# Kernel optimization log

Hardware: AMD Instinct MI355X
Metric: run time of the kernel (lower is better)

## Reference

```python
import jax, jax.numpy as jnp
import numpy as np

N = 100000      # nodes
E = 1600000     # edges
NG = 512        # graphs in batch
FIN = 7         # in_features
HID = 128       # hidden_channels
OUT = 2         # outfeatures


def setup_inputs() -> dict:
    key = jax.random.key(0)
    ks = jax.random.split(key, 16)
    x = jax.random.normal(ks[0], (N, FIN), jnp.float32)
    edge_index = jax.random.randint(ks[1], (2, E), 0, N, dtype=jnp.int64)
    batch = jnp.sort(jax.random.randint(ks[2], (N,), 0, NG, dtype=jnp.int64))

    def lin_w(k, fan_in, fan_out):
        # glorot-ish init, scale irrelevant for correctness baseline
        return jax.random.normal(k, (fan_in, fan_out), jnp.float32) / np.sqrt(fan_in).astype(np.float32)

    W1 = lin_w(ks[3], FIN, HID); b1 = jnp.zeros((HID,), jnp.float32)
    W2 = lin_w(ks[4], HID, HID); b2 = jnp.zeros((HID,), jnp.float32)
    W3 = lin_w(ks[5], HID, HID); b3 = jnp.zeros((HID,), jnp.float32)
    W4 = lin_w(ks[6], HID, HID); b4 = jnp.zeros((HID,), jnp.float32)
    Wlin = lin_w(ks[7], HID, OUT); blin = jnp.zeros((OUT,), jnp.float32)
    return dict(x=x, edge_index=edge_index, batch=batch,
                W1=W1, b1=b1, W2=W2, b2=b2, W3=W3, b3=b3, W4=W4, b4=b4,
                Wlin=Wlin, blin=blin)


def gcn_conv(h, W, b, src, dst, n):
    # PyG GCNConv: h' = D^{-1/2} (A + I) D^{-1/2} (h W) + b
    # src/dst already include self-loops
    h = h @ W
    deg = jax.ops.segment_sum(jnp.ones(src.shape[0], h.dtype), dst, num_segments=n)
    dinv = jnp.where(deg > 0, jax.lax.rsqrt(deg), jnp.zeros_like(deg))
    norm = dinv[src] * dinv[dst]                       # [E+N]
    agg = jax.ops.segment_sum(norm[:, None] * h[src], dst, num_segments=n)
    return agg + b


def reference(x, edge_index, batch, W1, b1, W2, b2, W3, b3, W4, b4, Wlin, blin):
    loop = jnp.arange(N, dtype=edge_index.dtype)
    src = jnp.concatenate([edge_index[0], loop])       # add self-loops
    dst = jnp.concatenate([edge_index[1], loop])

    h = gcn_conv(x, W1, b1, src, dst, N)
    for W, b in ((W2, b2), (W3, b3), (W4, b4)):
        h = jax.nn.relu(h)
        h = gcn_conv(h, W, b, src, dst, N)

    # global mean pool per graph
    sums = jax.ops.segment_sum(h, batch, num_segments=NG)
    cnt = jax.ops.segment_sum(jnp.ones((N,), h.dtype), batch, num_segments=NG)
    pooled = sums / jnp.maximum(cnt, 1.0)[:, None]     # [NG, HID]

    # dropout is identity in eval mode
    return pooled @ Wlin + blin                        # [NG, OUT]
```

## Files before the change

### kernel.cpp

```cpp
#include <hip/hip_runtime.h>
#include <hip/hip_bf16.h>

#define N_NODES 100000
#define E_EDGES 1600000
#define NG 512
#define FIN 7
#define HID 128
#define NBUCK 782
#define NBLK_SC 256
#define CHUNK 6250
#define TLEN (NBUCK * NBLK_SC)
#define NCH 196
#define MMX_GRID 782
#define AGGW_GRID 25000
#define L1_GRID 25000

typedef __attribute__((ext_vector_type(8))) short bf16x8;
typedef __attribute__((ext_vector_type(4))) float f32x4;

__device__ __forceinline__ float bf_lo(unsigned int u) { return __uint_as_float(u << 16); }
__device__ __forceinline__ float bf_hi(unsigned int u) { return __uint_as_float(u & 0xffff0000u); }
__device__ __forceinline__ unsigned int f2bf_rne(float f) {
    unsigned int x = __float_as_uint(f);
    return (x + 0x7fffu + ((x >> 16) & 1u)) >> 16;
}
__device__ __forceinline__ unsigned int pack_bf2(float lo, float hi) {
    return f2bf_rne(lo) | (f2bf_rne(hi) << 16);
}


__global__ __launch_bounds__(256) void k_hist2(const int* __restrict__ eidx,
                                               int* __restrict__ table,
                                               const float* __restrict__ W4,
                                               const float* __restrict__ b4,
                                               const float* __restrict__ Wlin,
                                               const float* __restrict__ blin,
                                               float* __restrict__ Wc,
                                               float* __restrict__ bc,
                                               float* __restrict__ pooled,
                                               const float* __restrict__ W2,
                                               const float* __restrict__ W3,
                                               unsigned short* __restrict__ WT2,
                                               unsigned short* __restrict__ WT3) {
    __shared__ int h[NBUCK];
    int blk = blockIdx.x, t = threadIdx.x;
    if (blk >= NBLK_SC) {
        int r = blk - NBLK_SC;
        if (r < 64) {
            float4 z = {0.f, 0.f, 0.f, 0.f};
            *(float4*)&pooled[(r * 256 + t) * 4] = z;
        } else if (r == 64) {
            int k = t >> 1, o = t & 1;
            float acc = 0.f;
            for (int j = 0; j < HID; ++j) acc += W4[k * HID + j] * Wlin[j * 2 + o];
            Wc[k * 2 + o] = acc;
            if (k == 0) {
                float b = blin[o];
                for (int j = 0; j < HID; ++j) b += b4[j] * Wlin[j * 2 + o];
                bc[o] = b;
            }
        } else if (r < 129) {
            int idx = (r - 65) * 256 + t;
            int k = idx >> 7, n = idx & 127;
            WT2[n * 128 + k] = (unsigned short)f2bf_rne(W2[idx]);
        } else {
            int idx = (r - 129) * 256 + t;
            int k = idx >> 7, n = idx & 127;
            WT3[n * 128 + k] = (unsigned short)f2bf_rne(W3[idx]);
        }
        return;
    }
    for (int i = t; i < NBUCK; i += 256) h[i] = 0;
    __syncthreads();
    int e0 = blk * CHUNK, e1 = e0 + CHUNK;
    for (int e = e0 + t; e < e1; e += 256)
        atomicAdd(&h[eidx[E_EDGES + e] >> 7], 1);
    __syncthreads();
    for (int i = t; i < NBUCK; i += 256)
        table[i * NBLK_SC + blk] = h[i];
}

__global__ void k_blocksum(const int* __restrict__ table, int* __restrict__ partial) {
    __shared__ int s[256];
    int b = blockIdx.x, t = threadIdx.x;
    int base = b * 1024;
    int sum = 0;
    for (int i = t; i < 1024; i += 256) {
        int idx = base + i;
        sum += (idx < TLEN) ? table[idx] : 0;
    }
    s[t] = sum; __syncthreads();
    for (int st = 128; st > 0; st >>= 1) {
        if (t < st) s[t] += s[t + st];
        __syncthreads();
    }
    if (t == 0) partial[b] = s[0];
}

__global__ void k_scan_blk(int* __restrict__ partial, int* __restrict__ bucketBase,
                           int* __restrict__ rowptr) {
    __shared__ int s[256];
    int t = threadIdx.x;
    int v = (t < NCH) ? partial[t] : 0;
    s[t] = v; __syncthreads();
    for (int st = 1; st < 256; st <<= 1) {
        int a = (t >= st) ? s[t - st] : 0;
        __syncthreads();
        s[t] += a;
        __syncthreads();
    }
    if (t < NCH) partial[t] = s[t] - v;
    if (t == 0) { bucketBase[NBUCK] = E_EDGES; rowptr[N_NODES] = E_EDGES; }
}

__global__ void k_scan_final(int* __restrict__ table, const int* __restrict__ partial,
                             int* __restrict__ bucketBase) {
    __shared__ int s[1024];
    int b = blockIdx.x, t = threadIdx.x;
    int idx = b * 1024 + t;
    int v = (idx < TLEN) ? table[idx] : 0;
    s[t] = v; __syncthreads();
    for (int st = 1; st < 1024; st <<= 1) {
        int add = (t >= st) ? s[t - st] : 0;
        __syncthreads();
        s[t] += add;
        __syncthreads();
    }
    if (idx < TLEN) {
        int ex = partial[b] + s[t] - v;
        table[idx] = ex;
        if ((idx & (NBLK_SC - 1)) == 0) bucketBase[idx / NBLK_SC] = ex;
    }
}

__global__ __launch_bounds__(256) void k_scatter2(const int* __restrict__ eidx,
                                                  const int* __restrict__ table,
                                                  unsigned int* __restrict__ ebuf) {
    __shared__ int loff[NBUCK];
    int blk = blockIdx.x, t = threadIdx.x;
    for (int i = t; i < NBUCK; i += 256) loff[i] = table[i * NBLK_SC + blk];
    __syncthreads();
    int e0 = blk * CHUNK, e1 = e0 + CHUNK;
    for (int e = e0 + t; e < e1; e += 256) {
        int s = eidx[e];
        int d = eidx[E_EDGES + e];
        int p = atomicAdd(&loff[d >> 7], 1);
        ebuf[p] = ((unsigned int)(d & 127) << 17) | (unsigned int)s;
    }
}

__global__ __launch_bounds__(256) void k_bucket(const unsigned int* __restrict__ ebuf,
                                                const int* __restrict__ bucketBase,
                                                int* __restrict__ rowptr,
                                                float* __restrict__ dinv,
                                                int* __restrict__ col,
                                                const float* __restrict__ x,
                                                float* __restrict__ xs) {
    __shared__ int scnt[128], soff[128], scur[128];
    int b = blockIdx.x, t = threadIdx.x;
    int bbase = bucketBase[b], bend = bucketBase[b + 1];
    if (t < 128) { scnt[t] = 0; scur[t] = 0; }
    __syncthreads();
    for (int e = bbase + t; e < bend; e += 256) {
        unsigned int rec = ebuf[e];
        atomicAdd(&scnt[rec >> 17], 1);
    }
    __syncthreads();
    if (t < 128) soff[t] = scnt[t];
    __syncthreads();
    for (int st = 1; st < 128; st <<= 1) {
        int a = (t < 128 && t >= st) ? soff[t - st] : 0;
        __syncthreads();
        if (t < 128) soff[t] += a;
        __syncthreads();
    }
    float dval = 0.f;
    if (t < 128) {
        int ex = soff[t] - scnt[t];
        int node = b * 128 + t;
        if (node < N_NODES) {
            rowptr[node] = bbase + ex;
            dval = rsqrtf((float)(scnt[t] + 1));
            dinv[node] = dval;
        }
        soff[t] = ex;
    }
    __syncthreads();
    for (int e = bbase + t; e < bend; e += 256) {
        unsigned int rec = ebuf[e];
        int dl = rec >> 17;
        int s = rec & 0x1FFFF;
        int p = bbase + soff[dl] + atomicAdd(&scur[dl], 1);
        col[p] = s;
    }
    if (t < 128) {
        int node = b * 128 + t;
        if (node < N_NODES) {
            float4 v0, v1;
            v0.x = dval * x[node * 7 + 0];
            v0.y = dval * x[node * 7 + 1];
            v0.z = dval * x[node * 7 + 2];
            v0.w = dval * x[node * 7 + 3];
            v1.x = dval * x[node * 7 + 4];
            v1.y = dval * x[node * 7 + 5];
            v1.z = dval * x[node * 7 + 6];
            v1.w = 0.f;
            *(float4*)&xs[node * 8] = v0;
            *(float4*)&xs[node * 8 + 4] = v1;
        }
    }
}


__global__ __launch_bounds__(256) void k_l1(const float* __restrict__ xs,
                                            const float* __restrict__ W1,
                                            const float* __restrict__ b1,
                                            const int* __restrict__ rowptr,
                                            const int* __restrict__ col,
                                            const float* __restrict__ dinv,
                                            unsigned int* __restrict__ g1) {
    __shared__ float w1s[FIN * HID];
    __shared__ float b1s[HID];
    int t = threadIdx.x;
    for (int i = t; i < FIN * HID; i += 256) w1s[i] = W1[i];
    if (t < HID) b1s[t] = b1[t];
    __syncthreads();

    int lane = t & 63, wave = t >> 6;
    int g = lane >> 3, r = lane & 7;
    int node = blockIdx.x * 4 + wave;
    float di = dinv[node];
    float acc = (g == 0) ? xs[node * 8 + r] : 0.f;
    int e0 = rowptr[node], e1 = rowptr[node + 1];

    for (int base = e0; base < e1; base += 64) {
        int m = e1 - base; if (m > 64) m = 64;
        int cv = col[base + lane];
        int j = 0;
        for (; j + 8 <= m; j += 8) {
            int s = __shfl(cv, j + g);
            acc += xs[s * 8 + r];
        }
        if (j < m) {
            int jg = j + g;
            int idx = (jg < m) ? jg : j;
            int s = __shfl(cv, idx);
            float u = xs[s * 8 + r];
            if (jg < m) acc += u;
        }
    }
    acc += __shfl_xor(acc, 8);
    acc += __shfl_xor(acc, 16);
    acc += __shfl_xor(acc, 32);
    acc *= di;

    float av[FIN];
    #pragma unroll
    for (int k = 0; k < FIN; ++k) av[k] = __shfl(acc, k);
    float2 bb = *(const float2*)&b1s[2 * lane];
    float acc0 = bb.x, acc1 = bb.y;
    #pragma unroll
    for (int k = 0; k < FIN; ++k) {
        float2 w = *(const float2*)&w1s[k * HID + 2 * lane];
        acc0 += av[k] * w.x;
        acc1 += av[k] * w.y;
    }
    g1[(size_t)node * 64 + lane] = pack_bf2(di * fmaxf(acc0, 0.f), di * fmaxf(acc1, 0.f));
}


__global__ __launch_bounds__(256) void k_aggW(const unsigned int* __restrict__ gIn,
                                              unsigned int* __restrict__ gOut,
                                              const int* __restrict__ rowptr,
                                              const int* __restrict__ colv,
                                              const float* __restrict__ dinv) {
    int wid = (blockIdx.x * blockDim.x + threadIdx.x) >> 6;
    int lane = threadIdx.x & 63;
    if (wid >= N_NODES) return;
    int i = wid;
    float di = dinv[i];
    int e0 = rowptr[i], e1 = rowptr[i + 1];
    int cv = colv[e0 + lane];
    unsigned int v = gIn[(size_t)i * 64 + lane];
    float ax = bf_lo(v), ay = bf_hi(v);

    for (int base = e0; base < e1; base += 64) {
        int m = e1 - base; if (m > 64) m = 64;
        int cvn = cv;
        if (base + 64 < e1) cvn = colv[base + 64 + lane];
        int j = 0;
        for (; j + 7 < m; j += 8) {
            int s0 = __shfl(cv, j),     s1 = __shfl(cv, j + 1);
            int s2 = __shfl(cv, j + 2), s3 = __shfl(cv, j + 3);
            int s4 = __shfl(cv, j + 4), s5 = __shfl(cv, j + 5);
            int s6 = __shfl(cv, j + 6), s7 = __shfl(cv, j + 7);
            unsigned int u0 = gIn[(size_t)s0 * 64 + lane];
            unsigned int u1 = gIn[(size_t)s1 * 64 + lane];
            unsigned int u2 = gIn[(size_t)s2 * 64 + lane];
            unsigned int u3 = gIn[(size_t)s3 * 64 + lane];
            unsigned int u4 = gIn[(size_t)s4 * 64 + lane];
            unsigned int u5 = gIn[(size_t)s5 * 64 + lane];
            unsigned int u6 = gIn[(size_t)s6 * 64 + lane];
            unsigned int u7 = gIn[(size_t)s7 * 64 + lane];
            ax += bf_lo(u0); ay += bf_hi(u0);
            ax += bf_lo(u1); ay += bf_hi(u1);
            ax += bf_lo(u2); ay += bf_hi(u2);
            ax += bf_lo(u3); ay += bf_hi(u3);
            ax += bf_lo(u4); ay += bf_hi(u4);
            ax += bf_lo(u5); ay += bf_hi(u5);
            ax += bf_lo(u6); ay += bf_hi(u6);
            ax += bf_lo(u7); ay += bf_hi(u7);
        }
        for (; j + 3 < m; j += 4) {
            int s0 = __shfl(cv, j),     s1 = __shfl(cv, j + 1);
            int s2 = __shfl(cv, j + 2), s3 = __shfl(cv, j + 3);
            unsigned int u0 = gIn[(size_t)s0 * 64 + lane];
            unsigned int u1 = gIn[(size_t)s1 * 64 + lane];
            unsigned int u2 = gIn[(size_t)s2 * 64 + lane];
            unsigned int u3 = gIn[(size_t)s3 * 64 + lane];
            ax += bf_lo(u0); ay += bf_hi(u0);
            ax += bf_lo(u1); ay += bf_hi(u1);
            ax += bf_lo(u2); ay += bf_hi(u2);
            ax += bf_lo(u3); ay += bf_hi(u3);
        }
        for (; j < m; ++j) {
            int s0 = __shfl(cv, j);
            unsigned int u0 = gIn[(size_t)s0 * 64 + lane];
            ax += bf_lo(u0); ay += bf_hi(u0);
        }
        cv = cvn;
    }
    gOut[(size_t)i * 64 + lane] = pack_bf2(di * ax, di * ay);
}


__global__ __launch_bounds__(256) void k_mmx(const unsigned int* __restrict__ gIn,
                                             const unsigned short* __restrict__ WTg,
                                             const float* __restrict__ bias,
                                             const float* __restrict__ dinv,
                                             unsigned int* __restrict__ outg) {
    __shared__ unsigned short sbuf[128 * 136];
    int t = threadIdx.x;
    for (int i = t * 8; i < 128 * 128; i += 256 * 8) {
        int n = i >> 7, k = i & 127;
        uint4 val = *(const uint4*)(WTg + i);
        *(uint4*)(sbuf + n * 136 + k) = val;
    }

    int lane = t & 63, wave = t >> 6;
    int m = lane & 15, quad = lane >> 4;
    int nodeBase = blockIdx.x * 128 + wave * 32;
    const short* gs = (const short*)gIn;

    float bi[8];
    #pragma unroll
    for (int nt = 0; nt < 8; ++nt) bi[nt] = bias[nt * 16 + m];

    f32x4 acc[2][8];
    #pragma unroll
    for (int gi = 0; gi < 2; ++gi)
        #pragma unroll
        for (int nt = 0; nt < 8; ++nt)
            acc[gi][nt] = (f32x4){0.f, 0.f, 0.f, 0.f};

    __syncthreads();

    #pragma unroll
    for (int kc = 0; kc < 4; ++kc) {
        bf16x8 ah[2];
        #pragma unroll
        for (int gi = 0; gi < 2; ++gi) {
            int node = nodeBase + gi * 16 + m;
            bf16x8 h = {0, 0, 0, 0, 0, 0, 0, 0};
            if (node < N_NODES)
                h = *(const bf16x8*)(gs + (size_t)node * 128 + kc * 32 + quad * 8);
            ah[gi] = h;
        }
        #pragma unroll
        for (int nt = 0; nt < 8; ++nt) {
            bf16x8 b = *(const bf16x8*)(sbuf + (nt * 16 + m) * 136 + kc * 32 + quad * 8);
            #pragma unroll
            for (int gi = 0; gi < 2; ++gi)
                acc[gi][nt] = __builtin_amdgcn_mfma_f32_16x16x32_bf16(ah[gi], b, acc[gi][nt], 0, 0, 0);
        }
    }

    __syncthreads();
    #pragma unroll
    for (int gi = 0; gi < 2; ++gi)
        #pragma unroll
        for (int r = 0; r < 4; ++r) {
            int nl = wave * 32 + gi * 16 + quad * 4 + r;
            int node = blockIdx.x * 128 + nl;
            float di = (node < N_NODES) ? dinv[node] : 0.f;
            #pragma unroll
            for (int nt = 0; nt < 8; ++nt) {
                float vv = acc[gi][nt][r] + bi[nt];
                sbuf[nl * 132 + nt * 16 + m] = (unsigned short)f2bf_rne(di * fmaxf(vv, 0.f));
            }
        }
    __syncthreads();
    for (int i = t; i < 128 * 32; i += 256) {
        int nl = i >> 5, p = i & 31;
        int node = blockIdx.x * 128 + nl;
        if (node < N_NODES) {
            uint2 val = *(const uint2*)(sbuf + nl * 132 + p * 4);
            *(uint2*)&outg[(size_t)node * 64 + p * 2] = val;
        }
    }
}


__global__ __launch_bounds__(256) void k_poolsum(const unsigned int* __restrict__ aggB,
                                                 const int* __restrict__ batch,
                                                 float* __restrict__ pooled) {
    int wid = (blockIdx.x * blockDim.x + threadIdx.x) >> 6;
    int lane = threadIdx.x & 63;
    int n0 = wid * 16;
    if (n0 >= N_NODES) return;
    int n1 = n0 + 16; if (n1 > N_NODES) n1 = N_NODES;
    int curg = batch[n0];
    float ax = 0.f, ay = 0.f;
    for (int n = n0; n < n1; ++n) {
        int g = batch[n];
        if (g != curg) {
            atomicAdd(&pooled[curg * HID + 2 * lane], ax);
            atomicAdd(&pooled[curg * HID + 2 * lane + 1], ay);
            ax = 0.f; ay = 0.f; curg = g;
        }
        unsigned int u = aggB[(size_t)n * 64 + lane];
        ax += bf_lo(u); ay += bf_hi(u);
    }
    atomicAdd(&pooled[curg * HID + 2 * lane], ax);
    atomicAdd(&pooled[curg * HID + 2 * lane + 1], ay);
}


__global__ void k_head(const float* __restrict__ pooled, const int* __restrict__ batch,
                       const float* __restrict__ Wc, const float* __restrict__ bc,
                       const float* __restrict__ blin, float* __restrict__ out) {
    int wid = (blockIdx.x * blockDim.x + threadIdx.x) >> 6;
    int lane = threadIdx.x & 63;
    if (wid >= NG) return;
    int g = wid;
    int lo = 0, hi = N_NODES;
    while (lo < hi) { int mid = (lo + hi) >> 1; if (batch[mid] < g) lo = mid + 1; else hi = mid; }
    int start = lo;
    hi = N_NODES;
    while (lo < hi) { int mid = (lo + hi) >> 1; if (batch[mid] < g + 1) lo = mid + 1; else hi = mid; }
    int cnt = lo - start;
    float invc = (cnt > 0) ? 1.0f / (float)cnt : 0.f;
    float px = pooled[g * HID + 2 * lane] * invc;
    float py = pooled[g * HID + 2 * lane + 1] * invc;

    #pragma unroll
    for (int o = 0; o < 2; ++o) {
        float v = px * Wc[(2 * lane) * 2 + o] + py * Wc[(2 * lane + 1) * 2 + o];
        #pragma unroll
        for (int s = 32; s > 0; s >>= 1) v += __shfl_down(v, s);
        if (lane == 0) out[g * 2 + o] = (cnt > 0) ? (v + bc[o]) : blin[o];
    }
}


extern "C" void kernel_launch(void* const* d_in, const int* in_sizes, int n_in,
                              void* d_out, int out_size, void* d_ws, size_t ws_size,
                              hipStream_t stream) {
    const float* x    = (const float*)d_in[0];
    const int*   eidx = (const int*)d_in[1];
    const int*   batch= (const int*)d_in[2];
    const float* W1   = (const float*)d_in[3];
    const float* b1   = (const float*)d_in[4];
    const float* W2   = (const float*)d_in[5];
    const float* b2   = (const float*)d_in[6];
    const float* W3   = (const float*)d_in[7];
    const float* b3   = (const float*)d_in[8];
    const float* W4   = (const float*)d_in[9];
    const float* b4   = (const float*)d_in[10];
    const float* Wlin = (const float*)d_in[11];
    const float* blin = (const float*)d_in[12];
    float* out = (float*)d_out;

    char* ws = (char*)d_ws;
    size_t off = 0;
    auto carve = [&](size_t bytes) { char* p = ws + off; off = (off + bytes + 255) & ~(size_t)255; return p; };
    int*   rowptr    = (int*)carve((size_t)(N_NODES + 1) * 4);
    float* dinv      = (float*)carve((size_t)N_NODES * 4);
    int*   col       = (int*)carve((size_t)E_EDGES * 4);
    unsigned int* ebuf = (unsigned int*)carve((size_t)E_EDGES * 4);
    int*   table     = (int*)carve((size_t)TLEN * 4);
    int*   partial   = (int*)carve((size_t)NCH * 4);
    int*   bucketBase= (int*)carve((size_t)(NBUCK + 1) * 4);
    float* xs        = (float*)carve((size_t)N_NODES * 8 * 4);
    unsigned int* gA = (unsigned int*)carve((size_t)N_NODES * 64 * 4);
    unsigned int* gB = (unsigned int*)carve((size_t)N_NODES * 64 * 4);
    float* pooled    = (float*)carve((size_t)NG * HID * 4);
    float* Wc        = (float*)carve((size_t)HID * 2 * 4);
    float* bc        = (float*)carve(2 * 4);
    unsigned short* WT2 = (unsigned short*)carve((size_t)HID * HID * 2);
    unsigned short* WT3 = (unsigned short*)carve((size_t)HID * HID * 2);
    (void)ws_size; (void)n_in; (void)in_sizes; (void)out_size;

    const int BLK = 256;
    int gridPS = ((N_NODES + 15) / 16 * 64 + BLK - 1) / BLK;
    int gridHead = (NG * 64 + BLK - 1) / BLK;

    k_hist2<<<NBLK_SC + 193, BLK, 0, stream>>>(eidx, table, W4, b4, Wlin, blin,
                                               Wc, bc, pooled, W2, W3, WT2, WT3);
    k_blocksum<<<NCH, BLK, 0, stream>>>(table, partial);
    k_scan_blk<<<1, 256, 0, stream>>>(partial, bucketBase, rowptr);
    k_scan_final<<<NCH, 1024, 0, stream>>>(table, partial, bucketBase);
    k_scatter2<<<NBLK_SC, BLK, 0, stream>>>(eidx, table, ebuf);
    k_bucket<<<NBUCK, BLK, 0, stream>>>(ebuf, bucketBase, rowptr, dinv, col, x, xs);

    k_l1<<<L1_GRID, BLK, 0, stream>>>(xs, W1, b1, rowptr, col, dinv, gA);

    k_aggW<<<AGGW_GRID, BLK, 0, stream>>>(gA, gB, rowptr, col, dinv);
    k_mmx<<<MMX_GRID, BLK, 0, stream>>>(gB, WT2, b2, dinv, gA);
    k_aggW<<<AGGW_GRID, BLK, 0, stream>>>(gA, gB, rowptr, col, dinv);
    k_mmx<<<MMX_GRID, BLK, 0, stream>>>(gB, WT3, b3, dinv, gA);
    k_aggW<<<AGGW_GRID, BLK, 0, stream>>>(gA, gB, rowptr, col, dinv);

    k_poolsum<<<gridPS, BLK, 0, stream>>>(gB, batch, pooled);
    k_head<<<gridHead, BLK, 0, stream>>>(pooled, batch, Wc, bc, blin, out);
}
```

Baseline: 422.6 us.

## Project final layer to 2 outputs before aggregation, skipping full-width last aggregation

The last GCN aggregation, mean pooling and head are linear, so the final layer's features are first projected through the combined W4·Wlin matrix down to 2 values per node, and the sparse aggregation then runs on these 2-wide values instead of 128-wide rows. This removes one full 128-channel edge gather pass and the 128-wide pooling with its atomics, replacing them with a per-node projection and a cheap 2-wide gather with per-graph atomics. Summation order changes and the bf16 intermediate is used directly, so numerics differ slightly.

```diff
diff --git a/kernel.cpp b/kernel.cpp
--- a/kernel.cpp
+++ b/kernel.cpp
@@ -14,6 +14,8 @@
 #define MMX_GRID 782
 #define AGGW_GRID 25000
 #define L1_GRID 25000
+#define PROJ_GRID 25000
+#define AGG2_GRID 6250
 
 typedef __attribute__((ext_vector_type(8))) short bf16x8;
 typedef __attribute__((ext_vector_type(4))) float f32x4;
@@ -37,7 +39,7 @@
                                                const float* __restrict__ blin,
                                                float* __restrict__ Wc,
                                                float* __restrict__ bc,
-                                               float* __restrict__ pooled,
+                                               float* __restrict__ pooled2,
                                                const float* __restrict__ W2,
                                                const float* __restrict__ W3,
                                                unsigned short* __restrict__ WT2,
@@ -46,10 +48,9 @@
     int blk = blockIdx.x, t = threadIdx.x;
     if (blk >= NBLK_SC) {
         int r = blk - NBLK_SC;
-        if (r < 64) {
+        if (r == 0) {
             float4 z = {0.f, 0.f, 0.f, 0.f};
-            *(float4*)&pooled[(r * 256 + t) * 4] = z;
-        } else if (r == 64) {
+            *(float4*)&pooled2[t * 4] = z;
             int k = t >> 1, o = t & 1;
             float acc = 0.f;
             for (int j = 0; j < HID; ++j) acc += W4[k * HID + j] * Wlin[j * 2 + o];
@@ -59,12 +60,12 @@
                 for (int j = 0; j < HID; ++j) b += b4[j] * Wlin[j * 2 + o];
                 bc[o] = b;
             }
-        } else if (r < 129) {
-            int idx = (r - 65) * 256 + t;
+        } else if (r < 65) {
+            int idx = (r - 1) * 256 + t;
             int k = idx >> 7, n = idx & 127;
             WT2[n * 128 + k] = (unsigned short)f2bf_rne(W2[idx]);
         } else {
-            int idx = (r - 129) * 256 + t;
+            int idx = (r - 65) * 256 + t;
             int k = idx >> 7, n = idx & 127;
             WT3[n * 128 + k] = (unsigned short)f2bf_rne(W3[idx]);
         }
@@ -411,54 +412,75 @@
 }
 
 
-__global__ __launch_bounds__(256) void k_poolsum(const unsigned int* __restrict__ aggB,
-                                                 const int* __restrict__ batch,
-                                                 float* __restrict__ pooled) {
+__global__ __launch_bounds__(256) void k_proj(const unsigned int* __restrict__ gIn,
+                                              const float* __restrict__ Wc,
+                                              float2* __restrict__ ps) {
     int wid = (blockIdx.x * blockDim.x + threadIdx.x) >> 6;
     int lane = threadIdx.x & 63;
-    int n0 = wid * 16;
-    if (n0 >= N_NODES) return;
-    int n1 = n0 + 16; if (n1 > N_NODES) n1 = N_NODES;
-    int curg = batch[n0];
-    float ax = 0.f, ay = 0.f;
-    for (int n = n0; n < n1; ++n) {
-        int g = batch[n];
-        if (g != curg) {
-            atomicAdd(&pooled[curg * HID + 2 * lane], ax);
-            atomicAdd(&pooled[curg * HID + 2 * lane + 1], ay);
-            ax = 0.f; ay = 0.f; curg = g;
-        }
-        unsigned int u = aggB[(size_t)n * 64 + lane];
-        ax += bf_lo(u); ay += bf_hi(u);
-    }
-    atomicAdd(&pooled[curg * HID + 2 * lane], ax);
-    atomicAdd(&pooled[curg * HID + 2 * lane + 1], ay);
-}
-
-
-__global__ void k_head(const float* __restrict__ pooled, const int* __restrict__ batch,
-                       const float* __restrict__ Wc, const float* __restrict__ bc,
-                       const float* __restrict__ blin, float* __restrict__ out) {
-    int wid = (blockIdx.x * blockDim.x + threadIdx.x) >> 6;
-    int lane = threadIdx.x & 63;
-    if (wid >= NG) return;
-    int g = wid;
+    unsigned int u = gIn[(size_t)wid * 64 + lane];
+    float4 w = *(const float4*)&Wc[lane * 4];
+    float p0 = bf_lo(u) * w.x + bf_hi(u) * w.z;
+    float p1 = bf_lo(u) * w.y + bf_hi(u) * w.w;
+    #pragma unroll
+    for (int s = 1; s < 64; s <<= 1) {
+        p0 += __shfl_xor(p0, s);
+        p1 += __shfl_xor(p1, s);
+    }
+    if (lane == 0) { float2 o; o.x = p0; o.y = p1; ps[wid] = o; }
+}
+
+
+__global__ __launch_bounds__(256) void k_agg2(const float2* __restrict__ ps,
+                                              const int* __restrict__ rowptr,
+                                              const int* __restrict__ col,
+                                              const float* __restrict__ dinv,
+                                              const int* __restrict__ batch,
+                                              float* __restrict__ pooled2) {
+    int t = threadIdx.x;
+    int node = (blockIdx.x * 256 + t) >> 4;
+    int r = t & 15;
+    int e0 = rowptr[node], e1 = rowptr[node + 1];
+    float a0 = 0.f, a1 = 0.f;
+    for (int e = e0 + r; e < e1; e += 16) {
+        int s = col[e];
+        float2 pv = ps[s];
+        a0 += pv.x; a1 += pv.y;
+    }
+    #pragma unroll
+    for (int sh = 1; sh < 16; sh <<= 1) {
+        a0 += __shfl_xor(a0, sh);
+        a1 += __shfl_xor(a1, sh);
+    }
+    if (r == 0) {
+        float2 pn = ps[node];
+        float di = dinv[node];
+        a0 = di * (a0 + pn.x);
+        a1 = di * (a1 + pn.y);
+        int g = batch[node];
+        atomicAdd(&pooled2[g * 2], a0);
+        atomicAdd(&pooled2[g * 2 + 1], a1);
+    }
+}
+
+
+__global__ void k_head2(const float* __restrict__ pooled2, const int* __restrict__ batch,
+                        const float* __restrict__ bc, const float* __restrict__ blin,
+                        float* __restrict__ out) {
+    int g = blockIdx.x * 256 + threadIdx.x;
+    if (g >= NG) return;
     int lo = 0, hi = N_NODES;
     while (lo < hi) { int mid = (lo + hi) >> 1; if (batch[mid] < g) lo = mid + 1; else hi = mid; }
     int start = lo;
     hi = N_NODES;
     while (lo < hi) { int mid = (lo + hi) >> 1; if (batch[mid] < g + 1) lo = mid + 1; else hi = mid; }
     int cnt = lo - start;
-    float invc = (cnt > 0) ? 1.0f / (float)cnt : 0.f;
-    float px = pooled[g * HID + 2 * lane] * invc;
-    float py = pooled[g * HID + 2 * lane + 1] * invc;
-
-    #pragma unroll
-    for (int o = 0; o < 2; ++o) {
-        float v = px * Wc[(2 * lane) * 2 + o] + py * Wc[(2 * lane + 1) * 2 + o];
-        #pragma unroll
-        for (int s = 32; s > 0; s >>= 1) v += __shfl_down(v, s);
-        if (lane == 0) out[g * 2 + o] = (cnt > 0) ? (v + bc[o]) : blin[o];
+    if (cnt > 0) {
+        float invc = 1.0f / (float)cnt;
+        out[g * 2]     = pooled2[g * 2] * invc + bc[0];
+        out[g * 2 + 1] = pooled2[g * 2 + 1] * invc + bc[1];
+    } else {
+        out[g * 2]     = blin[0];
+        out[g * 2 + 1] = blin[1];
     }
 }
 
@@ -494,7 +516,8 @@
     float* xs        = (float*)carve((size_t)N_NODES * 8 * 4);
     unsigned int* gA = (unsigned int*)carve((size_t)N_NODES * 64 * 4);
     unsigned int* gB = (unsigned int*)carve((size_t)N_NODES * 64 * 4);
-    float* pooled    = (float*)carve((size_t)NG * HID * 4);
+    float2* ps       = (float2*)carve((size_t)N_NODES * 8);
+    float* pooled2   = (float*)carve((size_t)NG * 2 * 4);
     float* Wc        = (float*)carve((size_t)HID * 2 * 4);
     float* bc        = (float*)carve(2 * 4);
     unsigned short* WT2 = (unsigned short*)carve((size_t)HID * HID * 2);
@@ -502,11 +525,9 @@
     (void)ws_size; (void)n_in; (void)in_sizes; (void)out_size;
 
     const int BLK = 256;
-    int gridPS = ((N_NODES + 15) / 16 * 64 + BLK - 1) / BLK;
-    int gridHead = (NG * 64 + BLK - 1) / BLK;
-
-    k_hist2<<<NBLK_SC + 193, BLK, 0, stream>>>(eidx, table, W4, b4, Wlin, blin,
-                                               Wc, bc, pooled, W2, W3, WT2, WT3);
+
+    k_hist2<<<NBLK_SC + 129, BLK, 0, stream>>>(eidx, table, W4, b4, Wlin, blin,
+                                               Wc, bc, pooled2, W2, W3, WT2, WT3);
     k_blocksum<<<NCH, BLK, 0, stream>>>(table, partial);
     k_scan_blk<<<1, 256, 0, stream>>>(partial, bucketBase, rowptr);
     k_scan_final<<<NCH, 1024, 0, stream>>>(table, partial, bucketBase);
@@ -519,8 +540,8 @@
     k_mmx<<<MMX_GRID, BLK, 0, stream>>>(gB, WT2, b2, dinv, gA);
     k_aggW<<<AGGW_GRID, BLK, 0, stream>>>(gA, gB, rowptr, col, dinv);
     k_mmx<<<MMX_GRID, BLK, 0, stream>>>(gB, WT3, b3, dinv, gA);
-    k_aggW<<<AGGW_GRID, BLK, 0, stream>>>(gA, gB, rowptr, col, dinv);
-
-    k_poolsum<<<gridPS, BLK, 0, stream>>>(gB, batch, pooled);
-    k_head<<<gridHead, BLK, 0, stream>>>(pooled, batch, Wc, bc, blin, out);
-}
+
+    k_proj<<<PROJ_GRID, BLK, 0, stream>>>(gA, Wc, ps);
+    k_agg2<<<AGG2_GRID, BLK, 0, stream>>>(ps, rowptr, col, dinv, batch, pooled2);
+    k_head2<<<2, BLK, 0, stream>>>(pooled2, batch, bc, blin, out);
+}
```

After: 506.4 us. 19.9% more time.
